# Kernel optimization log

Measured on AMD Instinct MI355X. Metric: run time of the kernel, lower is better.

Reference implementation:

```python
import jax, jax.numpy as jnp
import numpy as np
from jax.scipy.special import i0

B, P = 2, 524288
N = (512, 512)            # uniform frequency grid
M = 4                     # window cutoff m (2M taps per dim)
SIGMA = 2.0
NGRID = tuple(2 * (int(SIGMA * Ni) // 2) for Ni in N)  # oversampled grid (1024, 1024)
BETA = tuple(float(np.pi * (2.0 - 1.0 / (ng / Ni))) for ng, Ni in zip(NGRID, N))


def _phi_hat_1d(Ni, ni, b):
    # Fourier coefficients of the Kaiser-Bessel window, k = -Ni/2 .. Ni/2-1
    k = jnp.arange(-Ni // 2, Ni // 2, dtype=jnp.float32)
    arg = jnp.sqrt(b * b - (2.0 * jnp.pi * k / ni) ** 2)
    return i0(M * arg) / ni


def _window_ft():
    # separable d-dim Fourier coefficient grid, shape [N1, N2] (== window.ft)
    c1 = _phi_hat_1d(N[0], NGRID[0], BETA[0])
    c2 = _phi_hat_1d(N[1], NGRID[1], BETA[1])
    return c1[:, None] * c2[None, :]


def _phi(t, ni, b):
    # Kaiser-Bessel window in time domain, support |t| <= M/ni
    u2 = M * M - (ni * t) ** 2
    u = jnp.sqrt(jnp.maximum(u2, 1e-12))
    return jnp.where(u2 > 0, jnp.sinh(b * u) / (jnp.pi * u), 0.0)


def setup_inputs() -> dict:
    key = jax.random.key(0)
    k1, k2 = jax.random.split(key)
    x = jax.random.uniform(k1, (B, P, 2), jnp.float32, -0.5, 0.5)  # points on torus
    f_hat = jax.random.normal(k2, (B, N[0], N[1], 2), jnp.float32)  # complex as [re,im]
    return {"x": x, "f_hat": f_hat}


def _nfft_forward(x, f_hat):
    # f(x_j) ~= sum_k f_hat[k] exp(-2 pi i <k, x_j>) via window-deconvolved oversampled FFT + local gather
    fh = (f_hat[..., 0] + 1j * f_hat[..., 1]).astype(jnp.complex64)  # [B, N1, N2]
    ft = _window_ft().astype(jnp.float32)
    gh = fh / ft                                                    # deconvolve
    p1 = (NGRID[0] - N[0]) // 2
    p2 = (NGRID[1] - N[1]) // 2
    gh = jnp.pad(gh, ((0, 0), (p1, p1), (p2, p2)))                  # centered zero-pad to n
    g = jnp.fft.fftn(jnp.fft.ifftshift(gh, axes=(-2, -1)), axes=(-2, -1))
    g = g / (NGRID[0] * NGRID[1])                                   # g_l = (1/n) sum_k gh_k e^{-2pi i kl/n}

    offs = jnp.arange(-M + 1, M + 1)                                # [2M]
    ws, idxs = [], []
    for d in range(2):
        nd = NGRID[d]
        xd = x[..., d]                                              # [B, P]
        l0 = jnp.floor(xd * nd).astype(jnp.int32)
        l = l0[..., None] + offs                                    # [B, P, 2M]
        t = xd[..., None] - l.astype(jnp.float32) / nd
        ws.append(_phi(t, nd, BETA[d]))
        idxs.append(jnp.mod(l, nd))

    g_flat = g.reshape(B, NGRID[0] * NGRID[1])
    acc = jnp.zeros((B, P), jnp.complex64)
    for i in range(2 * M):                                          # fixed 2m x 2m taps
        for j in range(2 * M):
            flat = idxs[0][..., i] * NGRID[1] + idxs[1][..., j]     # [B, P]
            gv = jnp.take_along_axis(g_flat, flat, axis=1)
            acc = acc + (ws[0][..., i] * ws[1][..., j]) * gv
    return jnp.stack([acc.real, acc.imag], axis=-1)                 # [B, P, 2]


def reference(x, f_hat):
    return _nfft_forward(x, f_hat)
```

## Files before the change

### kernel.cpp

```cpp
#include <hip/hip_runtime.h>

constexpr int   BATCH = 2;
constexpr int   NPTS  = 524288;
constexpr int   BINS  = 2048;
constexpr int   CAP   = 768;
constexpr float BETA  = 4.71238898038469f;
constexpr float PI_F  = 3.14159265358979f;

typedef float v2f __attribute__((ext_vector_type(2)));
typedef unsigned u32x2 __attribute__((ext_vector_type(2)));

#define PIDX(i) ((i) + ((i) >> 4))

constexpr size_t G1_OFF   = 0;
constexpr size_t GT_OFF   = (size_t)16 << 20;
constexpr size_t GF_OFF   = 0;
constexpr size_t GCNT_OFF = (size_t)32 << 20;
constexpr size_t PERM_OFF = GCNT_OFF + 8192;

__device__ __forceinline__ float i0f_large(float x) {
    float t = 3.75f / x;
    float p =  0.00392377f;
    p = p * t + -0.01647633f;
    p = p * t +  0.02635537f;
    p = p * t + -0.02057706f;
    p = p * t +  0.00916281f;
    p = p * t + -0.00157565f;
    p = p * t +  0.00225319f;
    p = p * t +  0.01328592f;
    p = p * t +  0.39894228f;
    return __expf(x) * rsqrtf(x) * p;
}

__device__ __forceinline__ v2f cmul4(v2f a, float4 t) {
    v2f lo = {t.x, t.y}, hi = {t.z, t.w};
    return a.x * lo + a.y * hi;
}
__device__ __forceinline__ v2f irot(v2f b) { return (v2f){-b.y, b.x}; }

__device__ __forceinline__ int digitrev4_10(int f) {
    unsigned r = __brev((unsigned)f) >> 22;
    return (int)(((r & 0x2AAu) >> 1) | ((r & 0x155u) << 1));
}

__device__ __forceinline__ void build_tw4(float4* T, int tid, int nthreads) {
    int off = 0, q = 256, sig = 1;
    #pragma unroll
    for (int st = 0; st < 5; ++st) {
        for (int m = tid; m < 3 * q; m += nthreads) {
            int sec = 0, j = m;
            if (j >= q) { sec++; j -= q; }
            if (j >= q) { sec++; j -= q; }
            float ang = (-2.0f * PI_F / 1024.0f) * (float)((sec + 1) * j * sig);
            float sw, cw;
            __sincosf(ang, &sw, &cw);
            T[off + m] = make_float4(cw, sw, -sw, cw);
        }
        off += 3 * q; q >>= 2; sig <<= 2;
    }
}

__device__ __forceinline__ void bfly4(v2f* s, const float4* T,
                                      int bt, int q, int off) {
    int j    = bt & (q - 1);
    int base = ((bt - j) << 2) + j;
    int p0 = PIDX(base), p1 = PIDX(base + q);
    int p2 = PIDX(base + 2 * q), p3 = PIDX(base + 3 * q);
    v2f a0 = s[p0], a1 = s[p1], a2 = s[p2], a3 = s[p3];
    v2f t0 = a0 + a2, t1 = a0 - a2, t2 = a1 + a3, t3 = a1 - a3;
    v2f r3 = irot(t3);
    s[p0] = t0 + t2;
    s[p1] = cmul4(t1 - r3, T[off + j]);
    s[p2] = cmul4(t0 - t2, T[off + q + j]);
    s[p3] = cmul4(t1 + r3, T[off + 2 * q + j]);
}

__global__ __launch_bounds__(256) void rows_and_bin(const v2f* __restrict__ fh,
                                                    v2f* __restrict__ g,
                                                    const v2f* __restrict__ x,
                                                    int* __restrict__ gcnt,
                                                    u32x2* __restrict__ perm) {
    __shared__ __align__(16) char smem[25072];
    int tid = threadIdx.x;

    if (blockIdx.x < 1024) {
        if (blockIdx.x == 0) {
            #pragma unroll
            for (int i = 0; i < 8; ++i)
                atomicExch(&gcnt[tid * 8 + i], 0);
        }
        v2f*    s = (v2f*)smem;
        float4* T = (float4*)(smem + 8704);
        int blk = blockIdx.x & 511;
        int b   = blockIdx.x >> 9;
        int row = (blk < 256) ? blk : blk + 512;
        int a1  = (row + 256) & 1023;

        build_tw4(T, tid, 256);

        float k1 = (float)(a1 - 256);
        float w1 = (2.0f * PI_F / 1024.0f) * k1;
        float c1 = i0f_large(4.0f * sqrtf(BETA * BETA - w1 * w1));

        const v2f* fr = fh + ((long)b << 18) + ((long)a1 << 9);

        float w2a = (2.0f * PI_F / 1024.0f) * (float)tid;
        float c2a = i0f_large(4.0f * sqrtf(BETA * BETA - w2a * w2a));
        float w2b = (2.0f * PI_F / 1024.0f) * (float)(tid - 256);
        float c2b = i0f_large(4.0f * sqrtf(BETA * BETA - w2b * w2b));

        v2f A = fr[tid + 256] * (1.0f / (c1 * c2a));
        v2f B = fr[tid]       * (1.0f / (c1 * c2b));

        __syncthreads();

        v2f rB = irot(B);
        s[PIDX(tid)]       = A + B;
        s[PIDX(tid + 256)] = cmul4(A + rB, T[tid]);
        s[PIDX(tid + 512)] = cmul4(A - B,  T[256 + tid]);
        s[PIDX(tid + 768)] = cmul4(A - rB, T[512 + tid]);

        int off = 768, q = 64;
        #pragma unroll
        for (int st = 0; st < 4; ++st) {
            __syncthreads();
            bfly4(s, T, tid, q, off);
            off += 3 * q; q >>= 2;
        }
        __syncthreads();

        v2f* base = g + ((long)b << 20) + ((long)row << 10);
        #pragma unroll
        for (int i = 0; i < 4; ++i) {
            int idx = tid + (i << 8);
            base[idx] = s[PIDX(digitrev4_10(idx))];
        }
    } else {
        int* h = (int*)smem;
        int bblk = blockIdx.x - 1024;
        for (int i = tid; i < BINS; i += 256) h[i] = 0;
        __syncthreads();

        int base = bblk * 4096;
        int tile[16];
        u32x2 rec[16];
        #pragma unroll
        for (int i = 0; i < 16; ++i) {
            int gid = base + tid + i * 256;
            v2f xv  = x[gid];
            float xs1 = xv.x * 1024.0f, xs2 = xv.y * 1024.0f;
            float fl1 = floorf(xs1),    fl2 = floorf(xs2);
            int c1 = ((int)fl1) & 1023, c2 = ((int)fl2) & 1023;
            tile[i] = ((gid >> 19) << 10) + ((c1 >> 5) << 5) + (c2 >> 5);
            unsigned fq1 = (unsigned)((xs1 - fl1) * 65536.0f);
            unsigned fq2 = (unsigned)((xs2 - fl2) * 65536.0f);
            rec[i].x = (unsigned)gid | ((unsigned)(c1 & 31) << 20)
                                     | ((unsigned)(c2 & 31) << 25);
            rec[i].y = fq1 | (fq2 << 16);
            atomicAdd(&h[tile[i]], 1);
        }
        __syncthreads();

        #pragma unroll
        for (int j = 0; j < 8; ++j) {
            int bi = tid + j * 256;
            int c  = h[bi];
            h[bi]  = c ? atomicAdd(&gcnt[bi], c) : 0;
        }
        __syncthreads();

        #pragma unroll
        for (int i = 0; i < 16; ++i) {
            int pos = atomicAdd(&h[tile[i]], 1);
            perm[tile[i] * CAP + pos] = rec[i];
        }
    }
}

__global__ __launch_bounds__(256) void transpose_g(const v2f* __restrict__ g1,
                                                   v2f* __restrict__ gT) {
    __shared__ v2f tile[64][65];
    int bid = blockIdx.x;
    int b   = bid >> 7;
    int t7  = bid & 127;
    int rg  = t7 >> 4;
    int cg  = t7 & 15;
    int r0  = ((rg < 4) ? rg : rg + 8) << 6;
    int c0  = cg << 6;
    const v2f* src = g1 + ((long)b << 20);
    v2f*       dst = gT + ((long)b << 20);
    int lw = threadIdx.x >> 6;
    int ll = threadIdx.x & 63;

    #pragma unroll
    for (int k = 0; k < 16; ++k) {
        int r = lw + (k << 2);
        tile[r][ll] = src[((long)(r0 + r) << 10) + c0 + ll];
    }
    __syncthreads();
    #pragma unroll
    for (int k = 0; k < 16; ++k) {
        int c = lw + (k << 2);
        dst[((long)(c0 + c) << 10) + r0 + ll] = tile[ll][c];
    }
}

__global__ __launch_bounds__(256) void fft_cols2(const v2f* __restrict__ gT,
                                                 v2f* __restrict__ gF) {
    __shared__ __align__(16) char smem[25072];
    v2f*    s = (v2f*)smem;
    float4* T = (float4*)(smem + 8704);
    int tid = threadIdx.x;
    int c   = blockIdx.x;
    int b   = blockIdx.y;

    build_tw4(T, tid, 256);

    const v2f* row = gT + ((long)b << 20) + ((long)c << 10);
    v2f A = row[tid];
    v2f B = row[tid + 768];

    __syncthreads();

    v2f rB = irot(B);
    s[PIDX(tid)]       = A + B;
    s[PIDX(tid + 256)] = cmul4(A + rB, T[tid]);
    s[PIDX(tid + 512)] = cmul4(A - B,  T[256 + tid]);
    s[PIDX(tid + 768)] = cmul4(A - rB, T[512 + tid]);

    int off = 768, q = 64;
    #pragma unroll
    for (int st = 0; st < 4; ++st) {
        __syncthreads();
        bfly4(s, T, tid, q, off);
        off += 3 * q; q >>= 2;
    }
    __syncthreads();

    v2f* o = gF + ((long)b << 20) + ((long)c << 10);
    #pragma unroll
    for (int i = 0; i < 4; ++i) {
        int idx = tid + (i << 8);
        o[idx] = s[PIDX(digitrev4_10(idx))];
    }
}

__global__ __launch_bounds__(256) void gather_binned(const v2f* __restrict__ gF,
                                                     const int* __restrict__ gcnt,
                                                     const u32x2* __restrict__ perm,
                                                     v2f* __restrict__ out) {
    __shared__ v2f patch[37 * 37];
    int tb = blockIdx.x;
    int b  = tb >> 10;
    int tt = tb & 1023;
    int tR = tt >> 5, tC = tt & 31;
    int R0 = (tR << 5) - 2, C0 = (tC << 5) - 2;
    const v2f* gb = gF + ((long)b << 20);

    for (int p = threadIdx.x; p < 37 * 37; p += 256) {
        int pa = p / 37, pb = p - pa * 37;
        int gc = (C0 + pa) & 1023, gr = (R0 + pb) & 1023;
        patch[p] = gb[(gc << 10) + gr];
    }
    __syncthreads();

    int cnt = gcnt[tb];
    if (cnt > CAP) cnt = CAP;
    int off0 = tb * CAP;
    for (int i = (int)threadIdx.x; i < cnt; i += 256) {
        u32x2 rec = perm[off0 + i];
        int gid = (int)(rec.x & 0xFFFFFu);
        int rr0 = (int)((rec.x >> 20) & 31u);
        int cc0 = (int)((rec.x >> 25) & 31u);
        float fr1 = (float)(rec.y & 0xFFFFu) * (1.0f / 65536.0f);
        float fr2 = (float)(rec.y >> 16)     * (1.0f / 65536.0f);

        float w1[6], w2[6];
        #pragma unroll
        for (int k = 0; k < 6; ++k) {
            float tv = fr1 - (float)(k - 2);
            float u2 = 16.0f - tv * tv;
            float ir = rsqrtf(u2);
            float z  = BETA * u2 * ir;
            w1[k] = __expf(z) * 0.159154943f * ir;
        }
        #pragma unroll
        for (int k = 0; k < 6; ++k) {
            float tv = fr2 - (float)(k - 2);
            float u2 = 16.0f - tv * tv;
            float ir = rsqrtf(u2);
            float z  = BETA * u2 * ir;
            w2[k] = __expf(z) * 0.159154943f * ir;
        }

        v2f acc = {0.0f, 0.0f};
        #pragma unroll
        for (int jj = 0; jj < 6; ++jj) {
            int pbase = (cc0 + jj) * 37 + rr0;
            v2f s = {0.0f, 0.0f};
            #pragma unroll
            for (int ii = 0; ii < 6; ++ii)
                s += w1[ii] * patch[pbase + ii];
            acc += w2[jj] * s;
        }
        out[gid] = acc;
    }
}

extern "C" void kernel_launch(void* const* d_in, const int* in_sizes, int n_in,
                              void* d_out, int out_size, void* d_ws, size_t ws_size,
                              hipStream_t stream) {
    const v2f* x  = (const v2f*)d_in[0];
    const v2f* fh = (const v2f*)d_in[1];
    char* ws = (char*)d_ws;
    v2f*    g1   = (v2f*)(ws + G1_OFF);
    v2f*    gT   = (v2f*)(ws + GT_OFF);
    v2f*    gF   = (v2f*)(ws + GF_OFF);
    int*    gcnt = (int*)(ws + GCNT_OFF);
    u32x2*  perm = (u32x2*)(ws + PERM_OFF);

    rows_and_bin <<<dim3(1280),        dim3(256), 0, stream>>>(fh, g1, x, gcnt, perm);
    transpose_g  <<<dim3(256),         dim3(256), 0, stream>>>(g1, gT);
    fft_cols2    <<<dim3(1024, BATCH), dim3(256), 0, stream>>>(gT, gF);
    gather_binned<<<dim3(BINS),        dim3(256), 0, stream>>>(gF, gcnt, perm, (v2f*)d_out);
}
```

Before: 115.4 us.

## Fuse transpose into column FFT by processing 16 strided columns per block

Removes the separate transpose kernel. The column FFT now reads the row-FFT output directly, 16 columns at a time with coalesced row accesses, and splits each 1024-point transform into 4 quarter sub-FFTs across blockIdx.y. Output is written in natural row-major layout, so the gather kernel's patch load and tap loop are re-indexed to match. This saves one full-grid read/write pass and a launch, at the cost of partially coalesced 128-byte segments and more shared-memory bank pressure.

```diff
diff --git a/kernel.cpp b/kernel.cpp
--- a/kernel.cpp
+++ b/kernel.cpp
@@ -13,8 +13,7 @@
 #define PIDX(i) ((i) + ((i) >> 4))
 
 constexpr size_t G1_OFF   = 0;
-constexpr size_t GT_OFF   = (size_t)16 << 20;
-constexpr size_t GF_OFF   = 0;
+constexpr size_t GF_OFF   = (size_t)16 << 20;
 constexpr size_t GCNT_OFF = (size_t)32 << 20;
 constexpr size_t PERM_OFF = GCNT_OFF + 8192;
 
@@ -41,6 +40,10 @@
 __device__ __forceinline__ int digitrev4_10(int f) {
     unsigned r = __brev((unsigned)f) >> 22;
     return (int)(((r & 0x2AAu) >> 1) | ((r & 0x155u) << 1));
+}
+__device__ __forceinline__ int digitrev4_8(int f) {
+    unsigned r = __brev((unsigned)f) >> 24;
+    return (int)(((r & 0xAAu) >> 1) | ((r & 0x55u) << 1));
 }
 
 __device__ __forceinline__ void build_tw4(float4* T, int tid, int nthreads) {
@@ -177,71 +180,79 @@
     }
 }
 
-__global__ __launch_bounds__(256) void transpose_g(const v2f* __restrict__ g1,
-                                                   v2f* __restrict__ gT) {
-    __shared__ v2f tile[64][65];
-    int bid = blockIdx.x;
-    int b   = bid >> 7;
-    int t7  = bid & 127;
-    int rg  = t7 >> 4;
-    int cg  = t7 & 15;
-    int r0  = ((rg < 4) ? rg : rg + 8) << 6;
-    int c0  = cg << 6;
-    const v2f* src = g1 + ((long)b << 20);
-    v2f*       dst = gT + ((long)b << 20);
-    int lw = threadIdx.x >> 6;
-    int ll = threadIdx.x & 63;
-
-    #pragma unroll
-    for (int k = 0; k < 16; ++k) {
-        int r = lw + (k << 2);
-        tile[r][ll] = src[((long)(r0 + r) << 10) + c0 + ll];
+constexpr int REG = 271;
+__global__ __launch_bounds__(256) void fft_cols_q(const v2f* __restrict__ g1,
+                                                  v2f* __restrict__ gF) {
+    __shared__ __align__(16) char smem[16 * REG * 8 + 256 * 16 + 255 * 16];
+    v2f*    sd = (v2f*)smem;
+    float4* T1 = (float4*)(smem + 16 * REG * 8);
+    float4* Tq = (float4*)(smem + 16 * REG * 8 + 4096);
+
+    int tid = threadIdx.x;
+    int qd  = blockIdx.y;
+    int b   = blockIdx.z;
+    int C0  = blockIdx.x << 4;
+    int c   = tid & 15;
+    const v2f* gb = g1 + ((long)b << 20);
+    v2f*       go = gF + ((long)b << 20);
+
+    {
+        float ang = (-2.0f * PI_F / 1024.0f) * (float)(qd * tid);
+        float sw, cw;
+        __sincosf(ang, &sw, &cw);
+        T1[tid] = make_float4(cw, sw, -sw, cw);
+    }
+    if (tid < 255) {
+        int sec, j, sig;
+        if (tid < 192)      { sec = tid / 64;        j = tid & 63;        sig = 4;   }
+        else if (tid < 240) { sec = (tid - 192) / 16; j = (tid - 192) & 15; sig = 16; }
+        else if (tid < 252) { sec = (tid - 240) / 4;  j = (tid - 240) & 3;  sig = 64; }
+        else                { sec = tid - 252;        j = 0;               sig = 256; }
+        float ang = (-2.0f * PI_F / 1024.0f) * (float)((sec + 1) * j * sig);
+        float sw, cw;
+        __sincosf(ang, &sw, &cw);
+        Tq[tid] = make_float4(cw, sw, -sw, cw);
+    }
+
+    v2f Av[16], Bv[16];
+    #pragma unroll
+    for (int it = 0; it < 16; ++it) {
+        int j = (tid >> 4) + (it << 4);
+        Av[it] = gb[((long)j << 10) + C0 + c];
+        Bv[it] = gb[((long)(768 + j) << 10) + C0 + c];
     }
     __syncthreads();
-    #pragma unroll
-    for (int k = 0; k < 16; ++k) {
-        int c = lw + (k << 2);
-        dst[((long)(c0 + c) << 10) + r0 + ll] = tile[ll][c];
-    }
-}
-
-__global__ __launch_bounds__(256) void fft_cols2(const v2f* __restrict__ gT,
-                                                 v2f* __restrict__ gF) {
-    __shared__ __align__(16) char smem[25072];
-    v2f*    s = (v2f*)smem;
-    float4* T = (float4*)(smem + 8704);
-    int tid = threadIdx.x;
-    int c   = blockIdx.x;
-    int b   = blockIdx.y;
-
-    build_tw4(T, tid, 256);
-
-    const v2f* row = gT + ((long)b << 20) + ((long)c << 10);
-    v2f A = row[tid];
-    v2f B = row[tid + 768];
-
+
+    v2f* reg = sd + c * REG;
+    #pragma unroll
+    for (int it = 0; it < 16; ++it) {
+        int j = (tid >> 4) + (it << 4);
+        v2f A = Av[it], B = Bv[it], y;
+        if      (qd == 0) y = A + B;
+        else if (qd == 1) y = cmul4(A + irot(B), T1[j]);
+        else if (qd == 2) y = cmul4(A - B,       T1[j]);
+        else              y = cmul4(A - irot(B), T1[j]);
+        reg[PIDX(j)] = y;
+    }
     __syncthreads();
 
-    v2f rB = irot(B);
-    s[PIDX(tid)]       = A + B;
-    s[PIDX(tid + 256)] = cmul4(A + rB, T[tid]);
-    s[PIDX(tid + 512)] = cmul4(A - B,  T[256 + tid]);
-    s[PIDX(tid + 768)] = cmul4(A - rB, T[512 + tid]);
-
-    int off = 768, q = 64;
+    int off = 0, q = 64;
     #pragma unroll
     for (int st = 0; st < 4; ++st) {
-        __syncthreads();
-        bfly4(s, T, tid, q, off);
+        #pragma unroll
+        for (int k = 0; k < 4; ++k) {
+            int col = (tid >> 6) + (k << 2);
+            bfly4(sd + col * REG, Tq, tid & 63, q, off);
+        }
+        __syncthreads();
         off += 3 * q; q >>= 2;
     }
-    __syncthreads();
-
-    v2f* o = gF + ((long)b << 20) + ((long)c << 10);
-    #pragma unroll
-    for (int i = 0; i < 4; ++i) {
-        int idx = tid + (i << 8);
-        o[idx] = s[PIDX(digitrev4_10(idx))];
+
+    #pragma unroll
+    for (int it = 0; it < 16; ++it) {
+        int mm = (tid >> 4) + (it << 4);
+        int f  = (mm << 2) + qd;
+        go[((long)f << 10) + C0 + c] = reg[PIDX(digitrev4_8(mm))];
     }
 }
 
@@ -258,9 +269,9 @@
     const v2f* gb = gF + ((long)b << 20);
 
     for (int p = threadIdx.x; p < 37 * 37; p += 256) {
-        int pa = p / 37, pb = p - pa * 37;
-        int gc = (C0 + pa) & 1023, gr = (R0 + pb) & 1023;
-        patch[p] = gb[(gc << 10) + gr];
+        int pr = p / 37, pc = p - pr * 37;
+        int gr = (R0 + pr) & 1023, gc = (C0 + pc) & 1023;
+        patch[p] = gb[(gr << 10) + gc];
     }
     __syncthreads();
 
@@ -295,13 +306,13 @@
 
         v2f acc = {0.0f, 0.0f};
         #pragma unroll
-        for (int jj = 0; jj < 6; ++jj) {
-            int pbase = (cc0 + jj) * 37 + rr0;
+        for (int ii = 0; ii < 6; ++ii) {
+            int pbase = (rr0 + ii) * 37 + cc0;
             v2f s = {0.0f, 0.0f};
             #pragma unroll
-            for (int ii = 0; ii < 6; ++ii)
-                s += w1[ii] * patch[pbase + ii];
-            acc += w2[jj] * s;
+            for (int jj = 0; jj < 6; ++jj)
+                s += w2[jj] * patch[pbase + jj];
+            acc += w1[ii] * s;
         }
         out[gid] = acc;
     }
@@ -314,13 +325,11 @@
     const v2f* fh = (const v2f*)d_in[1];
     char* ws = (char*)d_ws;
     v2f*    g1   = (v2f*)(ws + G1_OFF);
-    v2f*    gT   = (v2f*)(ws + GT_OFF);
     v2f*    gF   = (v2f*)(ws + GF_OFF);
     int*    gcnt = (int*)(ws + GCNT_OFF);
     u32x2*  perm = (u32x2*)(ws + PERM_OFF);
 
-    rows_and_bin <<<dim3(1280),        dim3(256), 0, stream>>>(fh, g1, x, gcnt, perm);
-    transpose_g  <<<dim3(256),         dim3(256), 0, stream>>>(g1, gT);
-    fft_cols2    <<<dim3(1024, BATCH), dim3(256), 0, stream>>>(gT, gF);
-    gather_binned<<<dim3(BINS),        dim3(256), 0, stream>>>(gF, gcnt, perm, (v2f*)d_out);
-}
+    rows_and_bin <<<dim3(1280),         dim3(256), 0, stream>>>(fh, g1, x, gcnt, perm);
+    fft_cols_q   <<<dim3(64, 4, BATCH), dim3(256), 0, stream>>>(g1, gF);
+    gather_binned<<<dim3(BINS),         dim3(256), 0, stream>>>(gF, gcnt, perm, (v2f*)d_out);
+}
```

Result: no change. 115.4 us (-0.0%).
